# Kernel tuning notes

Hardware: AMD Instinct MI355X
Metric: run time of the kernel (lower is better)

Reference implementation:

```python
import jax, jax.numpy as jnp
import numpy as np

C, N, KS = 64, 64, 3  # channels, spatial size, kernel size (matches init_kwargs)
B = 4


def identity_kernel(c, k):
    # 'full' identity kernel: delta at spatial center on the channel diagonal
    ker = np.zeros((c, c, k, k), np.float32)
    ker[np.arange(c), np.arange(c), k // 2, k // 2] = 1.0
    return jnp.asarray(ker)


def setup_inputs() -> dict:
    key = jax.random.key(0)
    k1, k2, k3 = jax.random.split(key, 3)
    conv_in = jax.random.normal(k1, (B, C, N, N), jnp.float32)
    # small kernel perturbation, as produced by a hypernetwork at near-init ('I + net')
    K = jax.random.normal(k2, (B, C, C, KS, KS), jnp.float32) * 0.05
    bias = jax.random.normal(k3, (B, C, 1, 1), jnp.float32)
    return {"conv_in": conv_in, "K": K, "bias": bias}


def _circ_conv_one(x, ker):
    # x: [c, n, n], ker: [co, ci, kh, kw]; circular-padded cross-correlation (torch conv2d semantics)
    p = KS // 2
    xp = jnp.pad(x, ((0, 0), (p, p), (p, p)), mode="wrap")
    out = jax.lax.conv_general_dilated(
        xp[None], ker, window_strides=(1, 1), padding="VALID",
        dimension_numbers=("NCHW", "OIHW", "NCHW"))
    return out[0]  # [c, n, n]


def reference(conv_in, K, bias):
    # kernel_init == 'I + net': add identity kernel
    Kfull = K + identity_kernel(C, KS)[None]  # [B, c, c, k, k]

    # batch spatial circular conv2D with per-sample kernels
    conv_out = jax.vmap(_circ_conv_one)(conv_in, Kfull) + bias  # [B, c, n, n]

    # spectral log-determinant of the circular conv operator:
    # embed kernel into n x n grid, FFT2 over space, then per-frequency c x c logdet.
    # (per-frequency phase factors from kernel centering have unit modulus, so
    #  log|det| is independent of the spatial alignment convention)
    Kpad = jnp.zeros((K.shape[0], C, C, N, N), K.dtype).at[..., :KS, :KS].set(Kfull)
    Khat = jnp.fft.fft2(Kpad)                    # [B, c, c, n, n] complex
    Khat = jnp.moveaxis(Khat, (1, 2), (3, 4))    # [B, n, n, c, c]
    _, logabsdet = jnp.linalg.slogdet(Khat)      # [B, n, n]
    logdet = jnp.sum(logabsdet, axis=(1, 2))     # [B]

    return conv_out, logdet
```

## Files before the change

kernel.cpp:

```cpp
#include <hip/hip_runtime.h>
#include <hip/hip_fp16.h>
#include <math.h>

#define TAU 0.5f

__device__ __forceinline__ int h2i(__half2 h) { int i; __builtin_memcpy(&i, &h, 4); return i; }
__device__ __forceinline__ __half2 i2h(int i) { __half2 h; __builtin_memcpy(&h, &i, 4); return h; }

#define UPD(SL, LV) {                                                     \
    __half2 P_ = i2h(LV);                                                 \
    __half2 t_ = __hfma2(nfre2, P_, a2[SL]);                              \
    a2[(SL) - 1] = __hfma2(fim2, __lowhigh2highlow(P_), t_); }

#define CHUNK(CH) {                                                       \
    int l0 = __builtin_amdgcn_readlane(h2i(a2[(CH) * 8 + 1]), p);         \
    int l1 = __builtin_amdgcn_readlane(h2i(a2[(CH) * 8 + 2]), p);         \
    int l2 = __builtin_amdgcn_readlane(h2i(a2[(CH) * 8 + 3]), p);         \
    int l3 = __builtin_amdgcn_readlane(h2i(a2[(CH) * 8 + 4]), p);         \
    int l4 = __builtin_amdgcn_readlane(h2i(a2[(CH) * 8 + 5]), p);         \
    int l5 = __builtin_amdgcn_readlane(h2i(a2[(CH) * 8 + 6]), p);         \
    int l6 = __builtin_amdgcn_readlane(h2i(a2[(CH) * 8 + 7]), p);         \
    int l7 = __builtin_amdgcn_readlane(h2i(a2[(CH) * 8 + 8]), p);         \
    UPD((CH) * 8 + 1, l0) UPD((CH) * 8 + 2, l1) UPD((CH) * 8 + 3, l2)     \
    UPD((CH) * 8 + 4, l3) UPD((CH) * 8 + 5, l4) UPD((CH) * 8 + 6, l5)     \
    UPD((CH) * 8 + 7, l6) UPD((CH) * 8 + 8, l7) }

#define PREFIX()                                                          \
    float fr0 = __low2float(a2[0]);                                       \
    float fi0 = __high2float(a2[0]);                                      \
    float mag = fmaf(fr0, fr0, fi0 * fi0);                                \
    unsigned long long candm = __ballot(active && (mag >= TAU));          \
    int p;                                                                \
    if (candm != 0ULL) {                                                  \
      p = __ffsll(candm) - 1;                                             \
    } else {                                                              \
      float mm = active ? mag : -1.0f;                                    \
      for (int off = 32; off > 0; off >>= 1)                              \
        mm = fmaxf(mm, __shfl_xor(mm, off));                              \
      unsigned long long mx = __ballot(active && (mag == mm));            \
      if (mx == 0ULL) mx = __ballot(active);                              \
      p = __ffsll(mx) - 1;                                                \
    }                                                                     \
    p &= 63;                                                              \
    bool isPiv = (r == p);                                                \
    pivmag = isPiv ? mag : pivmag;                                        \
    active = active && !isPiv;                                            \
    float magp = __int_as_float(                                          \
        __builtin_amdgcn_readlane(__float_as_int(mag), p));               \
    __half2 pivh = i2h(__builtin_amdgcn_readlane(h2i(a2[0]), p));         \
    float pr = __low2float(pivh);                                         \
    float pi = __high2float(pivh);                                        \
    float inv = __builtin_amdgcn_rcpf(magp);                              \
    float fre = (fr0 * pr + fi0 * pi) * inv;                              \
    float fim = (fi0 * pr - fr0 * pi) * inv;                              \
    __half2 nfre2 = __float2half2_rn(-fre);                               \
    __half2 fim2 = __halves2half2(__float2half_rn(fim),                   \
                                  __float2half_rn(-fim));

__global__ __launch_bounds__(256, 3) void fused_kernel(
    const float* __restrict__ x, const float* __restrict__ K,
    const float* __restrict__ bias, float* __restrict__ out,
    float* __restrict__ logdet) {
  __shared__ float smem[4928];
  int bid = blockIdx.x;
  int t = threadIdx.x;

  int key;
  if (bid < 256) {
    int b = bid >> 6, co = bid & 63;
    float* w = smem;
    float* tile = smem + 576;

    for (int i = t; i < 576; i += 256) {
      float vv = K[(size_t)((b * 64 + co) * 64) * 9 + i];
      if (i == co * 9 + 4) vv += 1.0f;
      w[i] = vv;
    }

    int ty = t >> 2;
    int tx = t & 3;
    int x0 = tx << 4;
    float bval = bias[b * 64 + co];
    float acc[16];
#pragma unroll
    for (int i = 0; i < 16; ++i) acc[i] = bval;

    const float* xb = x + (size_t)(b * 64) * 4096;
    for (int ci = 0; ci < 64; ++ci) {
      __syncthreads();
      const float4* xc4 = (const float4*)(xb + (size_t)ci * 4096);
#pragma unroll
      for (int j = 0; j < 4; ++j) {
        int i4 = t + 256 * j;
        int row = i4 >> 4;
        int col = (i4 & 15) << 2;
        float4 vv = xc4[i4];
        *(float4*)&tile[row * 68 + col] = vv;
      }
      __syncthreads();

      float w0 = w[ci * 9 + 0], w1 = w[ci * 9 + 1], w2 = w[ci * 9 + 2];
      float w3 = w[ci * 9 + 3], w4 = w[ci * 9 + 4], w5 = w[ci * 9 + 5];
      float w6 = w[ci * 9 + 6], w7 = w[ci * 9 + 7], w8 = w[ci * 9 + 8];

      int ym = ((ty - 1) & 63) * 68;
      int yc = ty * 68;
      int yp = ((ty + 1) & 63) * 68;
      float in0[18], in1[18], in2[18];
#pragma unroll
      for (int q = 0; q < 4; ++q) {
        float4 v0 = *(const float4*)&tile[ym + x0 + 4 * q];
        float4 v1 = *(const float4*)&tile[yc + x0 + 4 * q];
        float4 v2 = *(const float4*)&tile[yp + x0 + 4 * q];
        in0[1 + 4 * q] = v0.x; in0[2 + 4 * q] = v0.y; in0[3 + 4 * q] = v0.z; in0[4 + 4 * q] = v0.w;
        in1[1 + 4 * q] = v1.x; in1[2 + 4 * q] = v1.y; in1[3 + 4 * q] = v1.z; in1[4 + 4 * q] = v1.w;
        in2[1 + 4 * q] = v2.x; in2[2 + 4 * q] = v2.y; in2[3 + 4 * q] = v2.z; in2[4 + 4 * q] = v2.w;
      }
      in0[0]  = tile[ym + ((x0 - 1) & 63)];
      in0[17] = tile[ym + ((x0 + 16) & 63)];
      in1[0]  = tile[yc + ((x0 - 1) & 63)];
      in1[17] = tile[yc + ((x0 + 16) & 63)];
      in2[0]  = tile[yp + ((x0 - 1) & 63)];
      in2[17] = tile[yp + ((x0 + 16) & 63)];
#pragma unroll
      for (int px = 0; px < 16; ++px) {
        float a = acc[px];
        a = fmaf(w0, in0[px], a); a = fmaf(w1, in0[px + 1], a); a = fmaf(w2, in0[px + 2], a);
        a = fmaf(w3, in1[px], a); a = fmaf(w4, in1[px + 1], a); a = fmaf(w5, in1[px + 2], a);
        a = fmaf(w6, in2[px], a); a = fmaf(w7, in2[px + 1], a); a = fmaf(w8, in2[px + 2], a);
        acc[px] = a;
      }
    }

    float* op = out + (size_t)(b * 64 + co) * 4096 + ty * 64 + x0;
#pragma unroll
    for (int i = 0; i < 16; i += 4) {
      *(float4*)(op + i) = make_float4(acc[i], acc[i + 1], acc[i + 2], acc[i + 3]);
    }

    if (bid >= 2) return;
    key = 2048 + bid;
  } else {
    key = bid - 256;
  }

  int b = t >> 6;
  int r = t & 63;

  int u, v;
  if (key < 33) { u = 0; v = key; }
  else if (key < 2017) { int q = key - 33; u = 1 + (q >> 6); v = q & 63; }
  else { u = 32; v = key - 2017; }
  float weight = (((u & 31) == 0) && ((v & 31) == 0)) ? 1.0f : 2.0f;

  float Ar[3], Ai[3], Br[3], Bi[3];
  {
    const float k2pi = -6.283185307179586f / 64.0f;
    float su, cu, sv, cv;
    __sincosf(k2pi * (float)u, &su, &cu);
    __sincosf(k2pi * (float)v, &sv, &cv);
    Ar[0] = 1.0f; Ai[0] = 0.0f; Ar[1] = cu; Ai[1] = su;
    Ar[2] = cu * cu - su * su; Ai[2] = 2.0f * cu * su;
    Br[0] = 1.0f; Bi[0] = 0.0f; Br[1] = cv; Bi[1] = sv;
    Br[2] = cv * cv - sv * sv; Bi[2] = 2.0f * cv * sv;
  }
  float wr[9], wi[9];
#pragma unroll
  for (int kh = 0; kh < 3; ++kh)
#pragma unroll
    for (int kw = 0; kw < 3; ++kw) {
      wr[kh * 3 + kw] = Ar[kh] * Br[kw] - Ai[kh] * Bi[kw];
      wi[kh * 3 + kw] = Ar[kh] * Bi[kw] + Ai[kh] * Br[kw];
    }

  __half2 a2[65];
  const float4* Kp4 = (const float4*)(K + (size_t)(b * 64 + r) * 576);
#pragma unroll
  for (int g = 0; g < 16; ++g) {
    float f[36];
#pragma unroll
    for (int qq = 0; qq < 9; ++qq) {
      float4 vv = Kp4[g * 9 + qq];
      f[qq * 4 + 0] = vv.x; f[qq * 4 + 1] = vv.y; f[qq * 4 + 2] = vv.z; f[qq * 4 + 3] = vv.w;
    }
#pragma unroll
    for (int cc = 0; cc < 4; ++cc) {
      int c = g * 4 + cc;
      float re = 0.0f, im = 0.0f;
#pragma unroll
      for (int t9 = 0; t9 < 9; ++t9) {
        float kv = f[cc * 9 + t9];
        re = fmaf(kv, wr[t9], re);
        im = fmaf(kv, wi[t9], im);
      }
      if (c == r) { re += wr[4]; im += wi[4]; }
      a2[c] = __floats2half2_rn(re, im);
    }
  }
  a2[64] = __floats2half2_rn(0.0f, 0.0f);

  bool active = true;
  float pivmag = 1.0f;

#pragma unroll 1
  for (int k = 0; k < 7; ++k) {
    PREFIX()
    CHUNK(0) CHUNK(1) CHUNK(2) CHUNK(3) CHUNK(4) CHUNK(5) CHUNK(6) CHUNK(7)
  }
#pragma unroll 1
  for (int k = 0; k < 8; ++k) {
    PREFIX()
    CHUNK(0) CHUNK(1) CHUNK(2) CHUNK(3) CHUNK(4) CHUNK(5) CHUNK(6)
  }
#pragma unroll 1
  for (int k = 0; k < 8; ++k) {
    PREFIX()
    CHUNK(0) CHUNK(1) CHUNK(2) CHUNK(3) CHUNK(4) CHUNK(5)
  }
#pragma unroll 1
  for (int k = 0; k < 8; ++k) {
    PREFIX()
    CHUNK(0) CHUNK(1) CHUNK(2) CHUNK(3) CHUNK(4)
  }
#pragma unroll 1
  for (int k = 0; k < 8; ++k) {
    PREFIX()
    CHUNK(0) CHUNK(1) CHUNK(2) CHUNK(3)
  }
#pragma unroll 1
  for (int k = 0; k < 8; ++k) {
    PREFIX()
    CHUNK(0) CHUNK(1) CHUNK(2)
  }
#pragma unroll 1
  for (int k = 0; k < 8; ++k) {
    PREFIX()
    CHUNK(0) CHUNK(1)
  }
#pragma unroll 1
  for (int k = 0; k < 8; ++k) {
    PREFIX()
    CHUNK(0)
  }

  {
    float fr0 = __low2float(a2[0]);
    float fi0 = __high2float(a2[0]);
    if (active) pivmag = fmaf(fr0, fr0, fi0 * fi0);
  }

  float logsum = 0.5f * __logf(pivmag);
#pragma unroll
  for (int off = 32; off > 0; off >>= 1) logsum += __shfl_xor(logsum, off);
  if (r == 0) atomicAdd(&logdet[b], weight * logsum);
}

extern "C" void kernel_launch(void* const* d_in, const int* in_sizes, int n_in,
                              void* d_out, int out_size, void* d_ws, size_t ws_size,
                              hipStream_t stream) {
  const float* conv_in = (const float*)d_in[0];
  const float* K       = (const float*)d_in[1];
  const float* bias    = (const float*)d_in[2];
  float* out = (float*)d_out;
  float* logdet = out + 1048576;

  hipMemsetAsync(logdet, 0, 4 * sizeof(float), stream);
  fused_kernel<<<dim3(2304), dim3(256), 0, stream>>>(conv_in, K, bias, out, logdet);
}
```

Baseline: 306.3 us.

## Software-pipeline pivot selection with elimination chunks in the per-frequency LU loop

Each elimination step now updates only the first chunk of the row (which holds the next pivot column) before choosing the next pivot and its multipliers. The remaining chunks are updated afterwards with the current multipliers, and the new multipliers are rotated in at the end of the iteration. The aim is to overlap the serial ballot, readlane and reciprocal latency of pivot search with the independent half2 FMA work of the other chunks. The explicit final-pivot epilogue is folded into the last pipelined prefix. This costs a few extra live registers for the next-step pivot state.

```diff
diff --git a/kernel.cpp b/kernel.cpp
--- a/kernel.cpp
+++ b/kernel.cpp
@@ -25,37 +25,39 @@
     UPD((CH) * 8 + 4, l3) UPD((CH) * 8 + 5, l4) UPD((CH) * 8 + 6, l5)     \
     UPD((CH) * 8 + 7, l6) UPD((CH) * 8 + 8, l7) }
 
-#define PREFIX()                                                          \
+#define PREFIX_CORE() {                                                   \
     float fr0 = __low2float(a2[0]);                                       \
     float fi0 = __high2float(a2[0]);                                      \
     float mag = fmaf(fr0, fr0, fi0 * fi0);                                \
     unsigned long long candm = __ballot(active && (mag >= TAU));          \
-    int p;                                                                \
+    int p_;                                                               \
     if (candm != 0ULL) {                                                  \
-      p = __ffsll(candm) - 1;                                             \
+      p_ = __ffsll(candm) - 1;                                            \
     } else {                                                              \
       float mm = active ? mag : -1.0f;                                    \
       for (int off = 32; off > 0; off >>= 1)                              \
         mm = fmaxf(mm, __shfl_xor(mm, off));                              \
       unsigned long long mx = __ballot(active && (mag == mm));            \
       if (mx == 0ULL) mx = __ballot(active);                              \
-      p = __ffsll(mx) - 1;                                                \
+      p_ = __ffsll(mx) - 1;                                               \
     }                                                                     \
-    p &= 63;                                                              \
-    bool isPiv = (r == p);                                                \
+    p_ &= 63;                                                             \
+    bool isPiv = (r == p_);                                               \
     pivmag = isPiv ? mag : pivmag;                                        \
     active = active && !isPiv;                                            \
     float magp = __int_as_float(                                          \
-        __builtin_amdgcn_readlane(__float_as_int(mag), p));               \
-    __half2 pivh = i2h(__builtin_amdgcn_readlane(h2i(a2[0]), p));         \
+        __builtin_amdgcn_readlane(__float_as_int(mag), p_));              \
+    __half2 pivh = i2h(__builtin_amdgcn_readlane(h2i(a2[0]), p_));        \
     float pr = __low2float(pivh);                                         \
     float pi = __high2float(pivh);                                        \
     float inv = __builtin_amdgcn_rcpf(magp);                              \
     float fre = (fr0 * pr + fi0 * pi) * inv;                              \
     float fim = (fi0 * pr - fr0 * pi) * inv;                              \
-    __half2 nfre2 = __float2half2_rn(-fre);                               \
-    __half2 fim2 = __halves2half2(__float2half_rn(fim),                   \
-                                  __float2half_rn(-fim));
+    pn = p_;                                                              \
+    nfre2n = __float2half2_rn(-fre);                                      \
+    fim2n = __halves2half2(__float2half_rn(fim), __float2half_rn(-fim)); }
+
+#define ROTATE() { p = pn; nfre2 = nfre2n; fim2 = fim2n; }
 
 __global__ __launch_bounds__(256, 3) void fused_kernel(
     const float* __restrict__ x, const float* __restrict__ K,
@@ -201,52 +203,66 @@
 
   bool active = true;
   float pivmag = 1.0f;
+  int p, pn;
+  __half2 nfre2, fim2, nfre2n, fim2n;
+
+  PREFIX_CORE()
+  ROTATE()
 
 #pragma unroll 1
   for (int k = 0; k < 7; ++k) {
-    PREFIX()
-    CHUNK(0) CHUNK(1) CHUNK(2) CHUNK(3) CHUNK(4) CHUNK(5) CHUNK(6) CHUNK(7)
-  }
-#pragma unroll 1
-  for (int k = 0; k < 8; ++k) {
-    PREFIX()
-    CHUNK(0) CHUNK(1) CHUNK(2) CHUNK(3) CHUNK(4) CHUNK(5) CHUNK(6)
-  }
-#pragma unroll 1
-  for (int k = 0; k < 8; ++k) {
-    PREFIX()
-    CHUNK(0) CHUNK(1) CHUNK(2) CHUNK(3) CHUNK(4) CHUNK(5)
-  }
-#pragma unroll 1
-  for (int k = 0; k < 8; ++k) {
-    PREFIX()
-    CHUNK(0) CHUNK(1) CHUNK(2) CHUNK(3) CHUNK(4)
-  }
-#pragma unroll 1
-  for (int k = 0; k < 8; ++k) {
-    PREFIX()
-    CHUNK(0) CHUNK(1) CHUNK(2) CHUNK(3)
-  }
-#pragma unroll 1
-  for (int k = 0; k < 8; ++k) {
-    PREFIX()
-    CHUNK(0) CHUNK(1) CHUNK(2)
-  }
-#pragma unroll 1
-  for (int k = 0; k < 8; ++k) {
-    PREFIX()
-    CHUNK(0) CHUNK(1)
-  }
-#pragma unroll 1
-  for (int k = 0; k < 8; ++k) {
-    PREFIX()
-    CHUNK(0)
-  }
-
-  {
-    float fr0 = __low2float(a2[0]);
-    float fi0 = __high2float(a2[0]);
-    if (active) pivmag = fmaf(fr0, fr0, fi0 * fi0);
+    CHUNK(0)
+    PREFIX_CORE()
+    CHUNK(1) CHUNK(2) CHUNK(3) CHUNK(4) CHUNK(5) CHUNK(6) CHUNK(7)
+    ROTATE()
+  }
+#pragma unroll 1
+  for (int k = 0; k < 8; ++k) {
+    CHUNK(0)
+    PREFIX_CORE()
+    CHUNK(1) CHUNK(2) CHUNK(3) CHUNK(4) CHUNK(5) CHUNK(6)
+    ROTATE()
+  }
+#pragma unroll 1
+  for (int k = 0; k < 8; ++k) {
+    CHUNK(0)
+    PREFIX_CORE()
+    CHUNK(1) CHUNK(2) CHUNK(3) CHUNK(4) CHUNK(5)
+    ROTATE()
+  }
+#pragma unroll 1
+  for (int k = 0; k < 8; ++k) {
+    CHUNK(0)
+    PREFIX_CORE()
+    CHUNK(1) CHUNK(2) CHUNK(3) CHUNK(4)
+    ROTATE()
+  }
+#pragma unroll 1
+  for (int k = 0; k < 8; ++k) {
+    CHUNK(0)
+    PREFIX_CORE()
+    CHUNK(1) CHUNK(2) CHUNK(3)
+    ROTATE()
+  }
+#pragma unroll 1
+  for (int k = 0; k < 8; ++k) {
+    CHUNK(0)
+    PREFIX_CORE()
+    CHUNK(1) CHUNK(2)
+    ROTATE()
+  }
+#pragma unroll 1
+  for (int k = 0; k < 8; ++k) {
+    CHUNK(0)
+    PREFIX_CORE()
+    CHUNK(1)
+    ROTATE()
+  }
+#pragma unroll 1
+  for (int k = 0; k < 8; ++k) {
+    CHUNK(0)
+    PREFIX_CORE()
+    ROTATE()
   }
 
   float logsum = 0.5f * __logf(pivmag);
```

Result: slower. 765.0 us (+149.8%).
